# Optimization experiments

Hardware: AMD Instinct MI355X
Metric: run time of the kernel (lower is better)

## Reference

```python
import jax, jax.numpy as jnp
import numpy as np

MODEL_DIM = 1024
NUM_HEADS = 16
HEAD_DIM = MODEL_DIM // NUM_HEADS
B, N = 4, 2048


def setup_inputs() -> dict:
    key = jax.random.key(0)
    ks = jax.random.split(key, 6)
    s = 1.0 / np.sqrt(MODEL_DIM)
    x = jax.random.normal(ks[0], (B, N, MODEL_DIM), dtype=jnp.float32)
    Wq = jax.random.uniform(ks[1], (MODEL_DIM, MODEL_DIM), jnp.float32, -s, s)
    Wk = jax.random.uniform(ks[2], (MODEL_DIM, MODEL_DIM), jnp.float32, -s, s)
    Wv = jax.random.uniform(ks[3], (MODEL_DIM, MODEL_DIM), jnp.float32, -s, s)
    Wo = jax.random.uniform(ks[4], (MODEL_DIM, MODEL_DIM), jnp.float32, -s, s)
    bo = jax.random.uniform(ks[5], (MODEL_DIM,), jnp.float32, -s, s)
    return {"x": x, "Wq": Wq, "Wk": Wk, "Wv": Wv, "Wo": Wo, "bo": bo}


def reference(x, Wq, Wk, Wv, Wo, bo):
    # QKV projections (no bias), split heads: b n (h d) -> b h n d
    def split(t):
        b, n, _ = t.shape
        return t.reshape(b, n, NUM_HEADS, HEAD_DIM).transpose(0, 2, 1, 3)

    q = split(x @ Wq.T)
    k = split(x @ Wk.T)
    v = split(x @ Wv.T)

    scale = HEAD_DIM ** (-0.5)
    scores = jnp.einsum('bhnd,bhmd->bhnm', q, k) * scale  # [B,H,N,N]
    # causal mask (is_causal=True)
    causal = jnp.tril(jnp.ones((N, N), dtype=bool))
    scores = jnp.where(causal, scores, -jnp.inf)
    attn = jax.nn.softmax(scores, axis=-1)
    out = jnp.einsum('bhnm,bhmd->bhnd', attn, v)  # [B,H,N,D]
    out = out.transpose(0, 2, 1, 3).reshape(B, N, MODEL_DIM)
    return out @ Wo.T + bo
```

## Files before the change

kernel.cpp:

```cpp
#include <hip/hip_runtime.h>
#include <hip/hip_bf16.h>

typedef unsigned short u16;
typedef __attribute__((ext_vector_type(8))) __bf16 bf16x8;
typedef __attribute__((ext_vector_type(4))) float f32x4;
typedef __attribute__((ext_vector_type(2))) unsigned int u32x2;

#define MODEL_DIM 1024
#define NUM_HEADS 16
#define HEAD_DIM  64
#define BATCH     4
#define SEQ       2048
#define ROWS      (BATCH*SEQ)

static __device__ __forceinline__ u16 f2bf(float f) {
    union { __hip_bfloat16 h; u16 u; } cv;
    cv.h = __float2bfloat16(f);
    return cv.u;
}

static __device__ __forceinline__ void gload16(const u16* g, unsigned lds_byte) {
    __builtin_amdgcn_global_load_lds(
        (const __attribute__((address_space(1))) unsigned int*)g,
        (__attribute__((address_space(3))) unsigned int*)(uintptr_t)lds_byte,
        16, 0, 0);
}

__global__ void castk_all(const float* __restrict__ x,
                          const float* __restrict__ w0, const float* __restrict__ w1,
                          const float* __restrict__ w2, const float* __restrict__ w3,
                          u16* __restrict__ out) {
    const int total = ROWS * MODEL_DIM + 4 * MODEL_DIM * MODEL_DIM;
    int i = (blockIdx.x * blockDim.x + threadIdx.x) * 4;
    int stride = gridDim.x * blockDim.x * 4;
    for (; i < total; i += stride) {
        const float* src;
        int off;
        if (i < ROWS * MODEL_DIM) { src = x; off = i; }
        else {
            int j = i - ROWS * MODEL_DIM;
            int w = j >> 20;
            off = j & 1048575;
            src = (w == 0) ? w0 : (w == 1) ? w1 : (w == 2) ? w2 : w3;
        }
        float4 v = *reinterpret_cast<const float4*>(src + off);
        ushort4 o;
        o.x = f2bf(v.x); o.y = f2bf(v.y); o.z = f2bf(v.z); o.w = f2bf(v.w);
        *reinterpret_cast<ushort4*>(out + i) = o;
    }
}


static __device__ __forceinline__ bf16x8 frag_read(const char* base, int row, int h,
                                                   int lo, int hi) {
    return *reinterpret_cast<const bf16x8*>(
        base + row * 128 + ((h * 64 + hi * 16) ^ ((lo & 7) << 4)));
}

template<int EPI>
__global__ __launch_bounds__(512, 2) void gemm_pipe(
    const u16* __restrict__ A,
    const u16* __restrict__ Wq, const u16* __restrict__ Wk, const u16* __restrict__ Wv,
    u16* __restrict__ qO, u16* __restrict__ kO, u16* __restrict__ vO,
    float* __restrict__ outF, const float* __restrict__ bias)
{
    __shared__ u16 As[2 * 16384];
    __shared__ u16 Bs[2 * 8192];
    const int t    = threadIdx.x;
    const int wid  = t >> 6;
    const int lane = t & 63;
    const int lo   = lane & 15, hi = lane >> 4;
    const int bm   = blockIdx.x * 256;
    int mat, bn;
    const u16* W;
    u16* outB = nullptr;
    float qscale = 1.0f;
    if (EPI == 0) {
        mat = blockIdx.y >> 3;
        bn  = (blockIdx.y & 7) * 128;
        W   = (mat == 0) ? Wq : (mat == 1) ? Wk : Wv;
        outB = (mat == 0) ? qO : (mat == 1) ? kO : vO;
        qscale = (mat == 0) ? 0.18033688f : 1.0f;
    } else {
        bn = blockIdx.y * 128;
        W  = Wq;
    }
    const int wr = wid >> 1, wc = wid & 1;
    const int K = MODEL_DIM;
    const unsigned AsB = (unsigned)(uintptr_t)As;
    const unsigned BsB = (unsigned)(uintptr_t)Bs;

    const u16* aSrc[4]; unsigned aDst[4];
    const u16* bSrc[2]; unsigned bDst[2];
#pragma unroll
    for (int ti = 0; ti < 4; ti++) {
        int o = t * 8 + ti * 4096;
        int row = o >> 6;
        int colb = ((o & 63) * 2) ^ ((row & 7) << 4);
        aSrc[ti] = A + (size_t)(bm + row) * K + (colb >> 1);
        aDst[ti] = (unsigned)(o * 2);
    }
#pragma unroll
    for (int ti = 0; ti < 2; ti++) {
        int o = t * 8 + ti * 4096;
        int row = o >> 6;
        int colb = ((o & 63) * 2) ^ ((row & 7) << 4);
        bSrc[ti] = W + (size_t)(bn + row) * K + (colb >> 1);
        bDst[ti] = (unsigned)(o * 2);
    }

    f32x4 acc[4][4];
#pragma unroll
    for (int m = 0; m < 4; m++)
#pragma unroll
        for (int n = 0; n < 4; n++) acc[m][n] = (f32x4){0.f, 0.f, 0.f, 0.f};

#pragma unroll
    for (int ti = 0; ti < 4; ti++) gload16(aSrc[ti], AsB + aDst[ti]);
#pragma unroll
    for (int ti = 0; ti < 2; ti++) gload16(bSrc[ti], BsB + bDst[ti]);

    for (int kt = 0; kt < 16; kt++) {
        const int p = kt & 1;
        if (kt < 15) {
            const int ko = (kt + 1) * 64;
            const unsigned pa = (unsigned)((p ^ 1) * 32768);
            const unsigned pb = (unsigned)((p ^ 1) * 16384);
#pragma unroll
            for (int ti = 0; ti < 4; ti++) gload16(aSrc[ti] + ko, AsB + pa + aDst[ti]);
#pragma unroll
            for (int ti = 0; ti < 2; ti++) gload16(bSrc[ti] + ko, BsB + pb + bDst[ti]);
            asm volatile("s_waitcnt vmcnt(6)" ::: "memory");
        } else {
            asm volatile("s_waitcnt vmcnt(0)" ::: "memory");
        }
        __builtin_amdgcn_s_barrier();
        __builtin_amdgcn_sched_barrier(0);

        const char* Ab = (const char*)As + p * 32768;
        const char* Bb = (const char*)Bs + p * 16384;
#pragma unroll
        for (int kk = 0; kk < 2; kk++) {
            bf16x8 bfr[4];
#pragma unroll
            for (int n = 0; n < 4; n++)
                bfr[n] = frag_read(Bb, wc * 64 + n * 16 + lo, kk, lo, hi);
#pragma unroll
            for (int mh = 0; mh < 2; mh++) {
                bf16x8 af[2];
#pragma unroll
                for (int m2 = 0; m2 < 2; m2++)
                    af[m2] = frag_read(Ab, wr * 64 + (mh * 2 + m2) * 16 + lo, kk, lo, hi);
                __builtin_amdgcn_s_setprio(1);
#pragma unroll
                for (int m2 = 0; m2 < 2; m2++)
#pragma unroll
                    for (int n = 0; n < 4; n++)
                        acc[mh * 2 + m2][n] = __builtin_amdgcn_mfma_f32_16x16x32_bf16(af[m2], bfr[n], acc[mh * 2 + m2][n], 0, 0, 0);
                __builtin_amdgcn_s_setprio(0);
                __builtin_amdgcn_s_barrier();
            }
        }
    }

#pragma unroll
    for (int m = 0; m < 4; m++)
#pragma unroll
        for (int n = 0; n < 4; n++)
#pragma unroll
            for (int r = 0; r < 4; r++) {
                int row = bm + wr * 64 + m * 16 + hi * 4 + r;
                int col = bn + wc * 64 + n * 16 + lo;
                if (EPI == 0) {
                    int b = row >> 11, np = row & 2047;
                    int hh = col >> 6, dd = col & 63;
                    outB[(((size_t)(b * NUM_HEADS + hh) * SEQ + np) << 6) + dd] = f2bf(acc[m][n][r] * qscale);
                } else {
                    outF[(size_t)row * MODEL_DIM + col] = acc[m][n][r] + bias[col];
                }
            }
}


static __device__ __forceinline__ u32x2 tr16(unsigned int addr) {
    u32x2 r;
    asm volatile("ds_read_b64_tr_b16 %0, %1" : "=v"(r) : "v"(addr));
    return r;
}

__global__ __launch_bounds__(256, 5) void attn(
    const u16* __restrict__ Q,
    const u16* __restrict__ Kg,
    const u16* __restrict__ Vg,
    u16* __restrict__ O)
{
    __shared__ u16 lds[16384];
    const int t    = threadIdx.x;
    const int wid  = t >> 6, lane = t & 63;
    const int lo   = lane & 15, hi = lane >> 4;

    const int g    = blockIdx.x;
    const int slot = g >> 3;
    const int bh   = ((slot & 7) << 3) + (g & 7);
    const int a    = slot >> 3;
    const int u    = a >> 2, a0 = a & 3;
    const int qt   = 4 * u + ((u & 1) ? 3 - a0 : a0);

    const size_t base = (size_t)bh * SEQ * 64;
    const int qbase = qt * 64 + wid * 16;
    const unsigned ldsb = (unsigned)(uintptr_t)lds;

    int srcK[2], srcV[2];
    unsigned dstK[2], dstV[2];
#pragma unroll
    for (int ti = 0; ti < 2; ti++) {
        int o   = t * 8 + ti * 2048;
        int row = o >> 6;
        int colb = ((o & 63) * 2) ^ ((row & 7) << 4);
        srcK[ti] = row * 64 + (colb >> 1);
        dstK[ti] = ldsb + o * 2;
        int st = o >> 9;
        int kv = (st >> 2) * 32 + ((o >> 4) & 31);
        int d  = (st & 3) * 16 + (o & 15);
        srcV[ti] = kv * 64 + d;
        dstV[ti] = ldsb + 8192u + o * 2;
    }

    bf16x8 qf[2];
#pragma unroll
    for (int h = 0; h < 2; h++)
        qf[h] = *reinterpret_cast<const bf16x8*>(Q + base + (size_t)(qbase + lo) * 64 + h * 32 + hi * 8);
    asm volatile("" : "+v"(qf[0]), "+v"(qf[1]));

    float m_run = -3.0e38f, l_part = 0.f;
    f32x4 acc[4];
#pragma unroll
    for (int dt = 0; dt < 4; dt++) acc[dt] = (f32x4){0.f, 0.f, 0.f, 0.f};

    {
        const u16* Kt = Kg + base;
        const u16* Vt = Vg + base;
#pragma unroll
        for (int ti = 0; ti < 2; ti++) {
            gload16(Kt + srcK[ti], dstK[ti]);
            gload16(Vt + srcV[ti], dstV[ti]);
        }
    }

    for (int j = 0; j <= qt; j++) {
        const int p = j & 1;
        if (j < qt) {
            const u16* Kt = Kg + base + (size_t)(j + 1) * 4096;
            const u16* Vt = Vg + base + (size_t)(j + 1) * 4096;
            const unsigned bs = (unsigned)((p ^ 1) * 16384);
#pragma unroll
            for (int ti = 0; ti < 2; ti++) {
                gload16(Kt + srcK[ti], dstK[ti] + bs);
                gload16(Vt + srcV[ti], dstV[ti] + bs);
            }
            asm volatile("s_waitcnt vmcnt(4)" ::: "memory");
        } else {
            asm volatile("s_waitcnt vmcnt(0)" ::: "memory");
        }
        __builtin_amdgcn_s_barrier();
        __builtin_amdgcn_sched_barrier(0);

        const char* Kcur = (const char*)lds + p * 16384;
        f32x4 s[4];
#pragma unroll
        for (int kh = 0; kh < 2; kh++) {
            bf16x8 kfa[2][2];
#pragma unroll
            for (int k2 = 0; k2 < 2; k2++)
#pragma unroll
                for (int h = 0; h < 2; h++)
                    kfa[k2][h] = *reinterpret_cast<const bf16x8*>(
                        Kcur + ((kh * 2 + k2) * 16 + lo) * 128 + ((h * 64 + hi * 16) ^ ((lo & 7) << 4)));
            __builtin_amdgcn_s_setprio(1);
#pragma unroll
            for (int k2 = 0; k2 < 2; k2++) {
                f32x4 a2 = (f32x4){0.f, 0.f, 0.f, 0.f};
#pragma unroll
                for (int h = 0; h < 2; h++)
                    a2 = __builtin_amdgcn_mfma_f32_16x16x32_bf16(kfa[k2][h], qf[h], a2, 0, 0, 0);
                s[kh * 2 + k2] = a2;
            }
            __builtin_amdgcn_s_setprio(0);
        }
        if (j == qt) {
            const int ql = wid * 16 + lo;
#pragma unroll
            for (int kt = 0; kt < 4; kt++)
#pragma unroll
                for (int r = 0; r < 4; r++)
                    if (kt * 16 + hi * 4 + r > ql) s[kt][r] = -1.0e30f;
        }
        float vm = s[0][0];
#pragma unroll
        for (int kt = 0; kt < 4; kt++)
#pragma unroll
            for (int r = 0; r < 4; r++) vm = fmaxf(vm, s[kt][r]);
        vm = fmaxf(vm, __shfl_xor(vm, 16));
        vm = fmaxf(vm, __shfl_xor(vm, 32));
        if (!__all(vm <= m_run + 8.0f)) {
            float nm = fmaxf(m_run, vm);
            float sc = exp2f(m_run - nm);
            m_run = nm;
            l_part *= sc;
#pragma unroll
            for (int dt = 0; dt < 4; dt++)
#pragma unroll
                for (int r = 0; r < 4; r++) acc[dt][r] *= sc;
        }
        float ps = 0.f;
#pragma unroll
        for (int kt = 0; kt < 4; kt++)
#pragma unroll
            for (int r = 0; r < 4; r++) {
                float pv = exp2f(s[kt][r] - m_run);
                s[kt][r] = pv;
                ps += pv;
            }
        l_part += ps;
        bf16x8 pa[2];
        {
            union { u16 uu[8]; bf16x8 v; } q0, q1;
#pragma unroll
            for (int e = 0; e < 4; e++) {
                q0.uu[e]     = f2bf(s[0][e]);
                q0.uu[4 + e] = f2bf(s[1][e]);
                q1.uu[e]     = f2bf(s[2][e]);
                q1.uu[4 + e] = f2bf(s[3][e]);
            }
            pa[0] = q0.v;
            pa[1] = q1.v;
        }

        const unsigned vtb = ldsb + (unsigned)(p * 16384) + 8192u + (unsigned)((hi * 64 + lo * 4) * 2);
#pragma unroll
        for (int pr = 0; pr < 2; pr++) {
            u32x2 tv[2][2][2];
#pragma unroll
            for (int d2 = 0; d2 < 2; d2++)
#pragma unroll
                for (int h = 0; h < 2; h++)
#pragma unroll
                    for (int sel = 0; sel < 2; sel++)
                        tv[d2][h][sel] = tr16(vtb + (unsigned)(((h * 4 + pr * 2 + d2) * 512 + sel * 256) * 2));
            asm volatile("s_waitcnt lgkmcnt(0)" ::: "memory");
            __builtin_amdgcn_sched_barrier(0);
            __builtin_amdgcn_s_setprio(1);
#pragma unroll
            for (int d2 = 0; d2 < 2; d2++) {
#pragma unroll
                for (int h = 0; h < 2; h++) {
                    union { unsigned int w[4]; bf16x8 v; } bv;
                    bv.w[0] = tv[d2][h][0][0];
                    bv.w[1] = tv[d2][h][0][1];
                    bv.w[2] = tv[d2][h][1][0];
                    bv.w[3] = tv[d2][h][1][1];
                    acc[pr * 2 + d2] = __builtin_amdgcn_mfma_f32_16x16x32_bf16(bv.v, pa[h], acc[pr * 2 + d2], 0, 0, 0);
                }
            }
            __builtin_amdgcn_s_setprio(0);
        }
        __builtin_amdgcn_s_barrier();
    }

    float l = l_part;
    l += __shfl_xor(l, 16);
    l += __shfl_xor(l, 32);
    const float inv = 1.0f / l;
    const int b = bh >> 4, hh = bh & 15;
    const size_t orow = ((size_t)(b * SEQ + qbase + lo)) * 1024 + hh * 64;
#pragma unroll
    for (int dt = 0; dt < 4; dt++) {
        union { u16 uu[4]; uint2 d2; } pk;
#pragma unroll
        for (int r = 0; r < 4; r++) pk.uu[r] = f2bf(acc[dt][r] * inv);
        *reinterpret_cast<uint2*>(O + orow + dt * 16 + hi * 4) = pk.d2;
    }
}

extern "C" void kernel_launch(void* const* d_in, const int* in_sizes, int n_in,
                              void* d_out, int out_size, void* d_ws, size_t ws_size,
                              hipStream_t stream) {
    const float* x  = (const float*)d_in[0];
    const float* Wq = (const float*)d_in[1];
    const float* Wk = (const float*)d_in[2];
    const float* Wv = (const float*)d_in[3];
    const float* Wo = (const float*)d_in[4];
    const float* bo = (const float*)d_in[5];
    float* out = (float*)d_out;

    char* ws = (char*)d_ws;
    u16* xb  = (u16*)ws;
    u16* wqb = (u16*)(ws + 16777216);
    u16* wkb = wqb + 1048576;
    u16* wvb = wkb + 1048576;
    u16* wob = wvb + 1048576;
    u16* q   = (u16*)(ws + 16777216 + 8388608);
    u16* k   = q + 8388608;
    u16* v   = k + 8388608;
    u16* ao  = v + 8388608;

    castk_all<<<3072, 256, 0, stream>>>(x, Wq, Wk, Wv, Wo, xb);

    gemm_pipe<0><<<dim3(ROWS / 256, 24), 512, 0, stream>>>(
        xb, wqb, wkb, wvb, q, k, v, nullptr, nullptr);

    attn<<<2048, 256, 0, stream>>>(q, k, v, ao);

    gemm_pipe<1><<<dim3(ROWS / 256, MODEL_DIM / 128), 512, 0, stream>>>(
        ao, wob, nullptr, nullptr, nullptr, nullptr, nullptr, out, bo);
}
```

Measured before the change: 175.0 us.

## Restructure attention pipeline: single-buffer V, row sums via MFMA, reverse tile order

Shrinks the attention kernel's LDS from 32KB to 24KB by double-buffering only K and loading V into a single buffer each iteration, with an extra barrier so V arrives while QK^T and softmax run. Raises launch bounds occupancy from 5 to 6 blocks. Computes softmax row sums with an MFMA against a ones vector instead of scalar adds and shuffles, and reverses the query-tile dispatch order so the longest causal tiles launch first. The extra barrier and the exposed V load latency may offset the occupancy gain.

After: 164.4 us. -6.1%, faster.

```diff
diff --git a/kernel.cpp b/kernel.cpp
--- a/kernel.cpp
+++ b/kernel.cpp
@@ -188,13 +188,13 @@
     return r;
 }
 
-__global__ __launch_bounds__(256, 5) void attn(
+__global__ __launch_bounds__(256, 6) void attn(
     const u16* __restrict__ Q,
     const u16* __restrict__ Kg,
     const u16* __restrict__ Vg,
     u16* __restrict__ O)
 {
-    __shared__ u16 lds[16384];
+    __shared__ u16 lds[12288];
     const int t    = threadIdx.x;
     const int wid  = t >> 6, lane = t & 63;
     const int lo   = lane & 15, hi = lane >> 4;
@@ -203,8 +203,9 @@
     const int slot = g >> 3;
     const int bh   = ((slot & 7) << 3) + (g & 7);
     const int a    = slot >> 3;
-    const int u    = a >> 2, a0 = a & 3;
-    const int qt   = 4 * u + ((u & 1) ? 3 - a0 : a0);
+    const int kq   = a >> 2, a0 = a & 3;
+    const int rk   = 7 - kq;
+    const int qt   = 4 * rk + ((rk & 1) ? 3 - a0 : a0);
 
     const size_t base = (size_t)bh * SEQ * 64;
     const int qbase = qt * 64 + wid * 16;
@@ -223,7 +224,7 @@
         int kv = (st >> 2) * 32 + ((o >> 4) & 31);
         int d  = (st & 3) * 16 + (o & 15);
         srcV[ti] = kv * 64 + d;
-        dstV[ti] = ldsb + 8192u + o * 2;
+        dstV[ti] = ldsb + 16384u + o * 2;
     }
 
     bf16x8 qf[2];
@@ -232,40 +233,45 @@
         qf[h] = *reinterpret_cast<const bf16x8*>(Q + base + (size_t)(qbase + lo) * 64 + h * 32 + hi * 8);
     asm volatile("" : "+v"(qf[0]), "+v"(qf[1]));
 
-    float m_run = -3.0e38f, l_part = 0.f;
-    f32x4 acc[4];
+    bf16x8 ones;
+    {
+        union { u16 uu[8]; bf16x8 v; } ov;
+#pragma unroll
+        for (int e = 0; e < 8; e++) ov.uu[e] = 0x3F80;
+        ones = ov.v;
+    }
+
+    float m_run = -3.0e38f;
+    f32x4 acc[4], lacc = (f32x4){0.f, 0.f, 0.f, 0.f};
 #pragma unroll
     for (int dt = 0; dt < 4; dt++) acc[dt] = (f32x4){0.f, 0.f, 0.f, 0.f};
+
+    const unsigned vtb = ldsb + 16384u + (unsigned)((hi * 64 + lo * 4) * 2);
 
     {
         const u16* Kt = Kg + base;
-        const u16* Vt = Vg + base;
-#pragma unroll
-        for (int ti = 0; ti < 2; ti++) {
-            gload16(Kt + srcK[ti], dstK[ti]);
-            gload16(Vt + srcV[ti], dstV[ti]);
-        }
+#pragma unroll
+        for (int ti = 0; ti < 2; ti++) gload16(Kt + srcK[ti], dstK[ti]);
+        asm volatile("s_waitcnt vmcnt(0)" ::: "memory");
     }
 
     for (int j = 0; j <= qt; j++) {
         const int p = j & 1;
-        if (j < qt) {
-            const u16* Kt = Kg + base + (size_t)(j + 1) * 4096;
-            const u16* Vt = Vg + base + (size_t)(j + 1) * 4096;
-            const unsigned bs = (unsigned)((p ^ 1) * 16384);
-#pragma unroll
-            for (int ti = 0; ti < 2; ti++) {
-                gload16(Kt + srcK[ti], dstK[ti] + bs);
-                gload16(Vt + srcV[ti], dstV[ti] + bs);
-            }
-            asm volatile("s_waitcnt vmcnt(4)" ::: "memory");
-        } else {
-            asm volatile("s_waitcnt vmcnt(0)" ::: "memory");
-        }
         __builtin_amdgcn_s_barrier();
+        {
+            const u16* Vt = Vg + base + (size_t)j * 4096;
+#pragma unroll
+            for (int ti = 0; ti < 2; ti++) gload16(Vt + srcV[ti], dstV[ti]);
+            if (j < qt) {
+                const u16* Kt = Kg + base + (size_t)(j + 1) * 4096;
+                const unsigned bs = (unsigned)((p ^ 1) * 8192);
+#pragma unroll
+                for (int ti = 0; ti < 2; ti++) gload16(Kt + srcK[ti], dstK[ti] + bs);
+            }
+        }
         __builtin_amdgcn_sched_barrier(0);
 
-        const char* Kcur = (const char*)lds + p * 16384;
+        const char* Kcur = (const char*)lds + p * 8192;
         f32x4 s[4];
 #pragma unroll
         for (int kh = 0; kh < 2; kh++) {
@@ -306,22 +312,17 @@
             float nm = fmaxf(m_run, vm);
             float sc = exp2f(m_run - nm);
             m_run = nm;
-            l_part *= sc;
+            lacc *= sc;
 #pragma unroll
             for (int dt = 0; dt < 4; dt++)
 #pragma unroll
                 for (int r = 0; r < 4; r++) acc[dt][r] *= sc;
         }
-        float ps = 0.f;
 #pragma unroll
         for (int kt = 0; kt < 4; kt++)
 #pragma unroll
-            for (int r = 0; r < 4; r++) {
-                float pv = exp2f(s[kt][r] - m_run);
-                s[kt][r] = pv;
-                ps += pv;
-            }
-        l_part += ps;
+            for (int r = 0; r < 4; r++)
+                s[kt][r] = exp2f(s[kt][r] - m_run);
         bf16x8 pa[2];
         {
             union { u16 uu[8]; bf16x8 v; } q0, q1;
@@ -335,8 +336,17 @@
             pa[0] = q0.v;
             pa[1] = q1.v;
         }
-
-        const unsigned vtb = ldsb + (unsigned)(p * 16384) + 8192u + (unsigned)((hi * 64 + lo * 4) * 2);
+        lacc = __builtin_amdgcn_mfma_f32_16x16x32_bf16(ones, pa[0], lacc, 0, 0, 0);
+        lacc = __builtin_amdgcn_mfma_f32_16x16x32_bf16(ones, pa[1], lacc, 0, 0, 0);
+
+        if (j < qt) {
+            asm volatile("s_waitcnt vmcnt(2)" ::: "memory");
+        } else {
+            asm volatile("s_waitcnt vmcnt(0)" ::: "memory");
+        }
+        __builtin_amdgcn_s_barrier();
+        __builtin_amdgcn_sched_barrier(0);
+
 #pragma unroll
         for (int pr = 0; pr < 2; pr++) {
             u32x2 tv[2][2][2];
@@ -364,13 +374,10 @@
             }
             __builtin_amdgcn_s_setprio(0);
         }
-        __builtin_amdgcn_s_barrier();
-    }
-
-    float l = l_part;
-    l += __shfl_xor(l, 16);
-    l += __shfl_xor(l, 32);
-    const float inv = 1.0f / l;
+        asm volatile("s_waitcnt vmcnt(0)" ::: "memory");
+    }
+
+    const float inv = 1.0f / lacc[0];
     const int b = bh >> 4, hh = bh & 15;
     const size_t orow = ((size_t)(b * SEQ + qbase + lo)) * 1024 + hh * 64;
 #pragma unroll
```
